# Kernel optimization log

Measured on AMD Instinct MI355X. Metric: run time of the kernel, lower is better.

## Reference

```python
import jax, jax.numpy as jnp
import numpy as np

# CycleFC1w1a constants (from init_kwargs / gen_offset)
IN_CH = 384
KH, KW = 1, 7  # cycle kernel; actual conv weight is 1x1
START = (KH * KW) // 2  # 3


def _gen_offset_x(C):
    # kernel_size[0] == 1 branch: off_y = 0, off_x[i] = (i + START) % KW - KW // 2
    i = jnp.arange(C)
    return (i + START) % KW - KW // 2  # int32, values in [-3, 3]


def setup_inputs() -> dict:
    key = jax.random.key(0)
    k1, k2, k3 = jax.random.split(key, 3)
    x = jax.random.normal(k1, (64, IN_CH, 32, 32), dtype=jnp.float32)
    weight = jax.random.normal(k2, (IN_CH, IN_CH), dtype=jnp.float32) * 0.05  # [out_ch, in_ch]
    bias = jax.random.normal(k3, (IN_CH,), dtype=jnp.float32) * 0.01
    return {"x": x, "weight": weight, "bias": bias}


def reference(x, weight, bias):
    B, C, H, W = x.shape
    # BinaryQuantizer forward: sign()
    xb = jnp.sign(x)
    wb = jnp.sign(weight)  # [O, C]

    # Fixed per-channel integer horizontal offsets -> exact shifted gather
    off_x = _gen_offset_x(C)                                  # [C]
    cols = jnp.arange(W)[None, :] + off_x[:, None]            # [C, W] sample col = w + off
    valid = (cols >= 0) & (cols < W)                          # zero-pad out of bounds
    cols_c = jnp.clip(cols, 0, W - 1)
    # gather along width per channel: [B, C, H, W]
    g = jnp.take_along_axis(xb, cols_c[None, :, None, :], axis=3)
    g = g * valid[None, :, None, :].astype(x.dtype)

    # pointwise (1x1) channel-mixing conv
    out = jnp.einsum('bchw,oc->bohw', g, wb) + bias[None, :, None, None]
    return out
```

## Files before the change

kernel.cpp:

```cpp
#include <hip/hip_runtime.h>
#include <stdint.h>


#define IN_CH 384
#define HH 32
#define WW 32
#define BB 64

constexpr uint64_t P7(int t) {
  uint64_t m = 0;
  for (int k = 0; k < 64; ++k)
    if (k % 7 == t) m |= (1ull << k);
  return m;
}
__device__ __constant__ uint64_t Pm[7] = {P7(0), P7(1), P7(2), P7(3), P7(4), P7(5), P7(6)};

__global__ __launch_bounds__(64) void cyc_prep(const float* __restrict__ wgt,
                                               const float* __restrict__ bias,
                                               uint64_t* __restrict__ wbg,
                                               float* __restrict__ bias2) {
  const int o = blockIdx.x;
  const int lane = threadIdx.x;
  __shared__ uint64_t wb_sh[6];
#pragma unroll
  for (int j = 0; j < 6; ++j) {
    uint64_t m = __ballot(wgt[o * IN_CH + j * 64 + lane] < 0.0f);
    if (lane == 0) wb_sh[j] = m;
  }
  __syncthreads();
  if (lane < 6) wbg[o * 6 + lane] = wb_sh[lane];
  if (lane < WW) {
    const int w = lane;
    int nv = 0, corr = 0;
#pragma unroll
    for (int j = 0; j < 6; ++j) {
      uint64_t V = 0;
#pragma unroll
      for (int d = -3; d <= 3; ++d) {
        int wd = w + d;
        if (wd >= 0 && wd < WW) V |= Pm[(d - j + 14) % 7];
      }
      nv += __popcll(V);
      corr += __popcll(wb_sh[j] & ~V);
    }
    bias2[o * WW + w] = bias[o] + (float)nv + 2.0f * (float)corr;
  }
}

__global__ __launch_bounds__(384) void cyc_main(const float* __restrict__ x,
                                                const uint64_t* __restrict__ wbg,
                                                const float* __restrict__ bias2,
                                                float* __restrict__ out) {
  __shared__ __align__(16) uint64_t sh_WB[IN_CH * 6];
  __shared__ uint64_t sh_X[WW][6];
  __shared__ uint64_t sh_G[WW][6];
  const int t = threadIdx.x;
  const int b = blockIdx.x >> 5;
  const int h = blockIdx.x & 31;

  {
    const float4* src = reinterpret_cast<const float4*>(wbg);
    float4* dst = reinterpret_cast<float4*>(sh_WB);
#pragma unroll
    for (int i = 0; i < 3; ++i) dst[t + i * 384] = src[t + i * 384];
  }

  const int wave = t >> 6, lane = t & 63;
  const int c = (wave << 6) + lane;
  const float4* xp =
      reinterpret_cast<const float4*>(x + (size_t)((b * IN_CH + c) * HH + h) * WW);
  unsigned myw = 0;
#pragma unroll
  for (int i = 0; i < 8; ++i) {
    float4 v = xp[i];
    myw |= (v.x < 0.0f ? 1u : 0u) << (i * 4 + 0);
    myw |= (v.y < 0.0f ? 1u : 0u) << (i * 4 + 1);
    myw |= (v.z < 0.0f ? 1u : 0u) << (i * 4 + 2);
    myw |= (v.w < 0.0f ? 1u : 0u) << (i * 4 + 3);
  }
#pragma unroll
  for (int w = 0; w < WW; ++w) {
    uint64_t m = __ballot((myw >> w) & 1u);
    if (lane == 0) sh_X[w][wave] = m;
  }
  __syncthreads();

  if (t < WW * 6) {
    const int w = t & 31, j = t >> 5;
    uint64_t g = 0;
#pragma unroll
    for (int d = -3; d <= 3; ++d) {
      int wd = w + d;
      if (wd >= 0 && wd < WW) g |= sh_X[wd][j] & Pm[(d - j + 14) % 7];
    }
    sh_G[w][j] = g;
  }
  __syncthreads();

  const int w = t & 31, og = t >> 5;
  const uint64_t g0 = sh_G[w][0], g1 = sh_G[w][1], g2 = sh_G[w][2];
  const uint64_t g3 = sh_G[w][3], g4 = sh_G[w][4], g5 = sh_G[w][5];
  float* op = out + (size_t)b * (IN_CH * HH * WW) + (size_t)(og * 32) * (HH * WW) +
              h * WW + w;
  const float* bp = bias2 + (og * 32) * WW + w;
  const ulonglong2* wv = reinterpret_cast<const ulonglong2*>(&sh_WB[(og * 32) * 6]);
#pragma unroll 4
  for (int i = 0; i < 32; ++i) {
    ulonglong2 q0 = wv[i * 3 + 0];
    ulonglong2 q1 = wv[i * 3 + 1];
    ulonglong2 q2 = wv[i * 3 + 2];
    int mm = __popcll(g0 ^ q0.x) + __popcll(g1 ^ q0.y) + __popcll(g2 ^ q1.x) +
             __popcll(g3 ^ q1.y) + __popcll(g4 ^ q2.x) + __popcll(g5 ^ q2.y);
    op[i * (HH * WW)] = bp[i * WW] - 2.0f * (float)mm;
  }
}

extern "C" void kernel_launch(void* const* d_in, const int* in_sizes, int n_in,
                              void* d_out, int out_size, void* d_ws, size_t ws_size,
                              hipStream_t stream) {
  const float* x = (const float*)d_in[0];
  const float* wgt = (const float*)d_in[1];
  const float* bias = (const float*)d_in[2];
  float* out = (float*)d_out;

  uint64_t* wbg = (uint64_t*)d_ws;
  float* bias2 = (float*)((char*)d_ws + IN_CH * 6 * sizeof(uint64_t));

  cyc_prep<<<IN_CH, 64, 0, stream>>>(wgt, bias, wbg, bias2);
  cyc_main<<<BB * HH, 384, 0, stream>>>(x, wbg, bias2, out);
}
```

Baseline: 216.4 us.

## Process four image rows per block to amortize weight staging and bias loads

Each block now handles four consecutive rows of one batch image instead of one, so the grid shrinks by a factor of four. The binarized weight table is copied into shared memory once per four rows, and each weight/bias load in the output loop is reused across four rows. Each thread also reads contiguous 512-byte spans of x. The cost is more registers (24 packed gate words) and fewer blocks, which may reduce occupancy and latency hiding on a memory-bound kernel.

```diff
diff --git a/kernel.cpp b/kernel.cpp
--- a/kernel.cpp
+++ b/kernel.cpp
@@ -47,16 +47,17 @@
   }
 }
 
+#define HR 4
 __global__ __launch_bounds__(384) void cyc_main(const float* __restrict__ x,
                                                 const uint64_t* __restrict__ wbg,
                                                 const float* __restrict__ bias2,
                                                 float* __restrict__ out) {
   __shared__ __align__(16) uint64_t sh_WB[IN_CH * 6];
-  __shared__ uint64_t sh_X[WW][6];
-  __shared__ uint64_t sh_G[WW][6];
+  __shared__ uint64_t sh_X[HR][WW][6];
+  __shared__ uint64_t sh_G[HR][WW][6];
   const int t = threadIdx.x;
-  const int b = blockIdx.x >> 5;
-  const int h = blockIdx.x & 31;
+  const int b = blockIdx.x >> 3;
+  const int h0 = (blockIdx.x & 7) * HR;
 
   {
     const float4* src = reinterpret_cast<const float4*>(wbg);
@@ -66,52 +67,72 @@
   }
 
   const int wave = t >> 6, lane = t & 63;
-  const int c = (wave << 6) + lane;
+  const int c = t;
   const float4* xp =
-      reinterpret_cast<const float4*>(x + (size_t)((b * IN_CH + c) * HH + h) * WW);
-  unsigned myw = 0;
+      reinterpret_cast<const float4*>(x + (size_t)((b * IN_CH + c) * HH + h0) * WW);
+  unsigned myw[HR];
 #pragma unroll
-  for (int i = 0; i < 8; ++i) {
-    float4 v = xp[i];
-    myw |= (v.x < 0.0f ? 1u : 0u) << (i * 4 + 0);
-    myw |= (v.y < 0.0f ? 1u : 0u) << (i * 4 + 1);
-    myw |= (v.z < 0.0f ? 1u : 0u) << (i * 4 + 2);
-    myw |= (v.w < 0.0f ? 1u : 0u) << (i * 4 + 3);
+  for (int r = 0; r < HR; ++r) {
+    unsigned m = 0;
+#pragma unroll
+    for (int i = 0; i < 8; ++i) {
+      float4 v = xp[r * 8 + i];
+      m |= (v.x < 0.0f ? 1u : 0u) << (i * 4 + 0);
+      m |= (v.y < 0.0f ? 1u : 0u) << (i * 4 + 1);
+      m |= (v.z < 0.0f ? 1u : 0u) << (i * 4 + 2);
+      m |= (v.w < 0.0f ? 1u : 0u) << (i * 4 + 3);
+    }
+    myw[r] = m;
   }
 #pragma unroll
-  for (int w = 0; w < WW; ++w) {
-    uint64_t m = __ballot((myw >> w) & 1u);
-    if (lane == 0) sh_X[w][wave] = m;
+  for (int r = 0; r < HR; ++r) {
+#pragma unroll
+    for (int w = 0; w < WW; ++w) {
+      uint64_t m = __ballot((myw[r] >> w) & 1u);
+      if (lane == 0) sh_X[r][w][wave] = m;
+    }
   }
   __syncthreads();
 
-  if (t < WW * 6) {
-    const int w = t & 31, j = t >> 5;
+#pragma unroll
+  for (int k = t; k < HR * WW * 6; k += 384) {
+    const int r = k / (WW * 6);
+    const int rem = k % (WW * 6);
+    const int w = rem & 31, j = rem >> 5;
     uint64_t g = 0;
 #pragma unroll
     for (int d = -3; d <= 3; ++d) {
       int wd = w + d;
-      if (wd >= 0 && wd < WW) g |= sh_X[wd][j] & Pm[(d - j + 14) % 7];
+      if (wd >= 0 && wd < WW) g |= sh_X[r][wd][j] & Pm[(d - j + 14) % 7];
     }
-    sh_G[w][j] = g;
+    sh_G[r][w][j] = g;
   }
   __syncthreads();
 
   const int w = t & 31, og = t >> 5;
-  const uint64_t g0 = sh_G[w][0], g1 = sh_G[w][1], g2 = sh_G[w][2];
-  const uint64_t g3 = sh_G[w][3], g4 = sh_G[w][4], g5 = sh_G[w][5];
+  uint64_t g[HR][6];
+#pragma unroll
+  for (int r = 0; r < HR; ++r)
+#pragma unroll
+    for (int j = 0; j < 6; ++j) g[r][j] = sh_G[r][w][j];
+
   float* op = out + (size_t)b * (IN_CH * HH * WW) + (size_t)(og * 32) * (HH * WW) +
-              h * WW + w;
+              h0 * WW + w;
   const float* bp = bias2 + (og * 32) * WW + w;
   const ulonglong2* wv = reinterpret_cast<const ulonglong2*>(&sh_WB[(og * 32) * 6]);
-#pragma unroll 4
+#pragma unroll 2
   for (int i = 0; i < 32; ++i) {
     ulonglong2 q0 = wv[i * 3 + 0];
     ulonglong2 q1 = wv[i * 3 + 1];
     ulonglong2 q2 = wv[i * 3 + 2];
-    int mm = __popcll(g0 ^ q0.x) + __popcll(g1 ^ q0.y) + __popcll(g2 ^ q1.x) +
-             __popcll(g3 ^ q1.y) + __popcll(g4 ^ q2.x) + __popcll(g5 ^ q2.y);
-    op[i * (HH * WW)] = bp[i * WW] - 2.0f * (float)mm;
+    float bb = bp[i * WW];
+#pragma unroll
+    for (int r = 0; r < HR; ++r) {
+      int mm = __popcll(g[r][0] ^ q0.x) + __popcll(g[r][1] ^ q0.y) +
+               __popcll(g[r][2] ^ q1.x) + __popcll(g[r][3] ^ q1.y) +
+               __popcll(g[r][4] ^ q2.x) + __popcll(g[r][5] ^ q2.y);
+      op[i * (HH * WW) + r * WW] = bb - 2.0f * (float)mm;
+    }
   }
 }
 
@@ -127,5 +148,5 @@
   float* bias2 = (float*)((char*)d_ws + IN_CH * 6 * sizeof(uint64_t));
 
   cyc_prep<<<IN_CH, 64, 0, stream>>>(wgt, bias, wbg, bias2);
-  cyc_main<<<BB * HH, 384, 0, stream>>>(x, wbg, bias2, out);
+  cyc_main<<<BB * (HH / HR), 384, 0, stream>>>(x, wbg, bias2, out);
 }
```

Result: faster. 210.8 us (-2.6%).

## Process two rows per block and read packed weights via scalar loads

Applied to the files above, without the earlier changes.

Each block now handles two image rows with 768 threads, halving the grid. The per-block copy of packed weights into shared memory is dropped. The weights are instead read straight from global memory with a wave-uniform output group (readfirstlane), so the loads can become scalar. Each wave writes 64 contiguous output floats covering two rows, which gives wider coalesced stores, at the cost of larger blocks and possible occupancy changes.

```diff
diff --git a/kernel.cpp b/kernel.cpp
--- a/kernel.cpp
+++ b/kernel.cpp
@@ -6,6 +6,7 @@
 #define HH 32
 #define WW 32
 #define BB 64
+#define HR 2
 
 constexpr uint64_t P7(int t) {
   uint64_t m = 0;
@@ -47,70 +48,70 @@
   }
 }
 
-__global__ __launch_bounds__(384) void cyc_main(const float* __restrict__ x,
+__global__ __launch_bounds__(768) void cyc_main(const float* __restrict__ x,
                                                 const uint64_t* __restrict__ wbg,
                                                 const float* __restrict__ bias2,
                                                 float* __restrict__ out) {
-  __shared__ __align__(16) uint64_t sh_WB[IN_CH * 6];
-  __shared__ uint64_t sh_X[WW][6];
-  __shared__ uint64_t sh_G[WW][6];
+  __shared__ uint64_t sh_X[HR][WW][6];
+  __shared__ uint64_t sh_G[HR][WW][6];
   const int t = threadIdx.x;
-  const int b = blockIdx.x >> 5;
-  const int h = blockIdx.x & 31;
+  const int b = blockIdx.x >> 4;
+  const int h0 = (blockIdx.x & 15) * HR;
+  const int wave = t >> 6, lane = t & 63;
 
   {
-    const float4* src = reinterpret_cast<const float4*>(wbg);
-    float4* dst = reinterpret_cast<float4*>(sh_WB);
+    const int j = wave % 6, r = wave / 6;
+    const int c = j * 64 + lane;
+    const float4* xp = reinterpret_cast<const float4*>(
+        x + (size_t)((b * IN_CH + c) * HH + h0 + r) * WW);
+    unsigned myw = 0;
 #pragma unroll
-    for (int i = 0; i < 3; ++i) dst[t + i * 384] = src[t + i * 384];
-  }
-
-  const int wave = t >> 6, lane = t & 63;
-  const int c = (wave << 6) + lane;
-  const float4* xp =
-      reinterpret_cast<const float4*>(x + (size_t)((b * IN_CH + c) * HH + h) * WW);
-  unsigned myw = 0;
+    for (int i = 0; i < 8; ++i) {
+      float4 v = xp[i];
+      myw |= (v.x < 0.0f ? 1u : 0u) << (i * 4 + 0);
+      myw |= (v.y < 0.0f ? 1u : 0u) << (i * 4 + 1);
+      myw |= (v.z < 0.0f ? 1u : 0u) << (i * 4 + 2);
+      myw |= (v.w < 0.0f ? 1u : 0u) << (i * 4 + 3);
+    }
 #pragma unroll
-  for (int i = 0; i < 8; ++i) {
-    float4 v = xp[i];
-    myw |= (v.x < 0.0f ? 1u : 0u) << (i * 4 + 0);
-    myw |= (v.y < 0.0f ? 1u : 0u) << (i * 4 + 1);
-    myw |= (v.z < 0.0f ? 1u : 0u) << (i * 4 + 2);
-    myw |= (v.w < 0.0f ? 1u : 0u) << (i * 4 + 3);
-  }
-#pragma unroll
-  for (int w = 0; w < WW; ++w) {
-    uint64_t m = __ballot((myw >> w) & 1u);
-    if (lane == 0) sh_X[w][wave] = m;
+    for (int w = 0; w < WW; ++w) {
+      uint64_t m = __ballot((myw >> w) & 1u);
+      if (lane == 0) sh_X[r][w][j] = m;
+    }
   }
   __syncthreads();
 
-  if (t < WW * 6) {
-    const int w = t & 31, j = t >> 5;
+  if (t < HR * WW * 6) {
+    const int r = t / (WW * 6);
+    const int q = t % (WW * 6);
+    const int w = q & 31, j = q >> 5;
     uint64_t g = 0;
 #pragma unroll
     for (int d = -3; d <= 3; ++d) {
       int wd = w + d;
-      if (wd >= 0 && wd < WW) g |= sh_X[wd][j] & Pm[(d - j + 14) % 7];
+      if (wd >= 0 && wd < WW) g |= sh_X[r][wd][j] & Pm[(d - j + 14) % 7];
     }
-    sh_G[w][j] = g;
+    sh_G[r][w][j] = g;
   }
   __syncthreads();
 
-  const int w = t & 31, og = t >> 5;
-  const uint64_t g0 = sh_G[w][0], g1 = sh_G[w][1], g2 = sh_G[w][2];
-  const uint64_t g3 = sh_G[w][3], g4 = sh_G[w][4], g5 = sh_G[w][5];
-  float* op = out + (size_t)b * (IN_CH * HH * WW) + (size_t)(og * 32) * (HH * WW) +
-              h * WW + w;
-  const float* bp = bias2 + (og * 32) * WW + w;
-  const ulonglong2* wv = reinterpret_cast<const ulonglong2*>(&sh_WB[(og * 32) * 6]);
+  const int og = __builtin_amdgcn_readfirstlane(wave);
+  const int w = lane & 31, r = lane >> 5;
+  uint64_t g0, g1, g2, g3, g4, g5;
+  {
+    const ulonglong2* gv = reinterpret_cast<const ulonglong2*>(&sh_G[r][w][0]);
+    ulonglong2 a = gv[0], bq = gv[1], cq = gv[2];
+    g0 = a.x; g1 = a.y; g2 = bq.x; g3 = bq.y; g4 = cq.x; g5 = cq.y;
+  }
+  float* op = out + ((size_t)b * IN_CH + og * 32) * (HH * WW) + h0 * WW + lane;
+  const uint64_t* wp = wbg + og * 32 * 6;
+  const float* bp = bias2 + og * 32 * WW + w;
 #pragma unroll 4
   for (int i = 0; i < 32; ++i) {
-    ulonglong2 q0 = wv[i * 3 + 0];
-    ulonglong2 q1 = wv[i * 3 + 1];
-    ulonglong2 q2 = wv[i * 3 + 2];
-    int mm = __popcll(g0 ^ q0.x) + __popcll(g1 ^ q0.y) + __popcll(g2 ^ q1.x) +
-             __popcll(g3 ^ q1.y) + __popcll(g4 ^ q2.x) + __popcll(g5 ^ q2.y);
+    const uint64_t w0 = wp[i * 6 + 0], w1 = wp[i * 6 + 1], w2 = wp[i * 6 + 2];
+    const uint64_t w3 = wp[i * 6 + 3], w4 = wp[i * 6 + 4], w5 = wp[i * 6 + 5];
+    int mm = __popcll(g0 ^ w0) + __popcll(g1 ^ w1) + __popcll(g2 ^ w2) +
+             __popcll(g3 ^ w3) + __popcll(g4 ^ w4) + __popcll(g5 ^ w5);
     op[i * (HH * WW)] = bp[i * WW] - 2.0f * (float)mm;
   }
 }
@@ -127,5 +128,5 @@
   float* bias2 = (float*)((char*)d_ws + IN_CH * 6 * sizeof(uint64_t));
 
   cyc_prep<<<IN_CH, 64, 0, stream>>>(wgt, bias, wbg, bias2);
-  cyc_main<<<BB * HH, 384, 0, stream>>>(x, wbg, bias2, out);
+  cyc_main<<<BB * (HH / HR), 768, 0, stream>>>(x, wbg, bias2, out);
 }
```

Measured after the change: 200.1 us. 7.5% less time.
